# Kernel optimization log

Hardware: AMD Instinct MI355X
Metric: run time of the kernel (lower is better)

The kernel has to match this reference:

```python
import math
import jax, jax.numpy as jnp
import numpy as np

N_KV = 8
GROUP = 4
HEAD_DIM = 128
BATCH = 512
CACHE = 2048
CONTEXT = 4096
NEG_INF = -10000.0


def setup_inputs() -> dict:
    key = jax.random.key(0)
    k = jax.random.split(key, 6)
    queries = jax.random.normal(k[0], (N_KV * GROUP, BATCH, HEAD_DIM), jnp.float32)
    keys = jax.random.normal(k[1], (N_KV, BATCH, HEAD_DIM), jnp.float32)
    key_t_caches = jax.random.normal(k[2], (N_KV, HEAD_DIM, CACHE), jnp.float32)
    values = jax.random.normal(k[3], (N_KV, BATCH, HEAD_DIM), jnp.float32)
    value_caches = jax.random.normal(k[4], (N_KV, CACHE, HEAD_DIM), jnp.float32)
    # causal bias: token b (global position CACHE+b) may attend to positions <= CACHE+b;
    # padded tail [CACHE+BATCH, CONTEXT) is always masked with NEG_INF
    pos = jnp.arange(CONTEXT)[None, :]                       # [1, CONTEXT]
    limit = (CACHE + jnp.arange(BATCH))[:, None]             # [BATCH, 1]
    attn_bias = jnp.where(pos <= limit, 0.0, NEG_INF).astype(jnp.float32)
    kq_scale = jnp.asarray([1.0 / math.sqrt(HEAD_DIM)], jnp.float32)
    return {
        "queries": queries,
        "keys": keys,
        "key_t_caches": key_t_caches,
        "values": values,
        "value_caches": value_caches,
        "attn_bias": attn_bias,
        "kq_scale": kq_scale,
    }


def reference(queries, keys, key_t_caches, values, value_caches, attn_bias, kq_scale):
    n_kv, B, D = keys.shape
    n_heads = queries.shape[0]
    group = n_heads // n_kv
    cache = key_t_caches.shape[-1]
    context = attn_bias.shape[-1]
    pad = context - cache - B

    scaled_keys = keys * kq_scale                            # [kv, B, D]
    scaled_values = jnp.maximum(values, NEG_INF)             # [kv, B, D]

    # pad new keys/values to fill context, then prepend cache (matches torch pad+cat)
    padded_kt = jnp.pad(scaled_keys.transpose(0, 2, 1), ((0, 0), (0, 0), (0, pad)))
    all_keys_t = jnp.concatenate([key_t_caches, padded_kt], axis=-1)   # [kv, D, context]
    padded_v = jnp.pad(scaled_values, ((0, 0), (0, pad), (0, 0)))
    all_values = jnp.concatenate([value_caches, padded_v], axis=1)     # [kv, context, D]

    q = queries.reshape(n_kv, group, B, D)                   # group-major per kv head
    scores = jnp.einsum('kgbd,kdc->kgbc', q, all_keys_t) + attn_bias   # [kv, g, B, context]
    probs = jax.nn.softmax(scores, axis=-1)
    out = jnp.einsum('kgbc,kcd->kgbd', probs, all_values)    # [kv, g, B, D]
    head_outs = out.reshape(n_heads, B, D)
    return head_outs, scaled_keys, scaled_values
```

## Files before the change

### kernel.cpp

```cpp
#include <hip/hip_runtime.h>
#include <hip/hip_bf16.h>

#define NKV 8
#define NHEADS 32
#define HDIM 128
#define BATCH 512
#define CACHE 2048
#define CTX_TOT 2560
#define CT 64
#define SPLITS 4
#define KPITCH 136
#define VPITCH 72
#define PPITCH 72
#define NEG_BIG (-1e30f)

typedef __attribute__((ext_vector_type(8))) _Float16 half8;
typedef __attribute__((ext_vector_type(4))) float floatx4;

__global__ __launch_bounds__(256) void prep(const float* __restrict__ ktc,
                                            const float* __restrict__ vc,
                                            const float* __restrict__ keys,
                                            const float* __restrict__ values,
                                            const float* __restrict__ kq,
                                            float* __restrict__ outk,
                                            float* __restrict__ outv,
                                            _Float16* __restrict__ Kh,
                                            _Float16* __restrict__ Vth) {
    __shared__ float tile[32][33];
    const int bid = blockIdx.x;
    const int t = threadIdx.x;
    const int x = t & 31, y = t >> 5;

    if (bid < 2048) {
        int l = bid;
        int c0 = (l & 63) * 32, d0 = ((l >> 6) & 3) * 32, kv = l >> 8;
        const float* src = ktc + ((size_t)kv * HDIM + d0) * CACHE + c0;
#pragma unroll
        for (int i = 0; i < 4; i++)
            tile[y + 8 * i][x] = src[(size_t)(y + 8 * i) * CACHE + x];
        __syncthreads();
        _Float16* dst = Kh + ((size_t)kv * CTX_TOT + c0) * HDIM + d0;
#pragma unroll
        for (int i = 0; i < 4; i++)
            dst[(size_t)(y + 8 * i) * HDIM + x] = (_Float16)tile[x][y + 8 * i];
    } else if (bid < 4096) {
        int l = bid - 2048;
        int c0 = (l & 63) * 32, d0 = ((l >> 6) & 3) * 32, kv = l >> 8;
        const float* src = vc + ((size_t)kv * CACHE + c0) * HDIM + d0;
#pragma unroll
        for (int i = 0; i < 4; i++)
            tile[y + 8 * i][x] = src[(size_t)(y + 8 * i) * HDIM + x];
        __syncthreads();
        _Float16* dst = Vth + ((size_t)kv * HDIM + d0) * CTX_TOT + c0;
#pragma unroll
        for (int i = 0; i < 4; i++)
            dst[(size_t)(y + 8 * i) * CTX_TOT + x] = (_Float16)tile[x][y + 8 * i];
    } else if (bid < 6144) {
        int i = (bid - 4096) * 256 + t;
        float s = kq[0];
        float v = keys[i] * s;
        outk[i] = v;
        int kv = i >> 16;
        int rem = i & 0xFFFF;
        Kh[((size_t)kv * CTX_TOT + CACHE) * HDIM + rem] = (_Float16)v;
    } else {
        int l = bid - 6144;
        int b0 = (l & 15) * 32, d0 = ((l >> 4) & 3) * 32, kv = l >> 6;
        const float* src = values + ((size_t)kv * BATCH + b0) * HDIM + d0;
        float* dst32 = outv + ((size_t)kv * BATCH + b0) * HDIM + d0;
#pragma unroll
        for (int i = 0; i < 4; i++) {
            float v = fmaxf(src[(size_t)(y + 8 * i) * HDIM + x], -10000.0f);
            tile[y + 8 * i][x] = v;
            dst32[(size_t)(y + 8 * i) * HDIM + x] = v;
        }
        __syncthreads();
        _Float16* dst = Vth + ((size_t)kv * HDIM + d0) * CTX_TOT + CACHE + b0;
#pragma unroll
        for (int i = 0; i < 4; i++)
            dst[(size_t)(y + 8 * i) * CTX_TOT + x] = (_Float16)tile[x][y + 8 * i];
    }
}

__global__ __launch_bounds__(256) void attn_split(const float* __restrict__ q_g,
                                                  const _Float16* __restrict__ Kh,
                                                  const _Float16* __restrict__ Vth,
                                                  float* __restrict__ Opart,
                                                  float* __restrict__ MLpart) {
    __shared__ _Float16 Klds[CT * KPITCH];
    __shared__ _Float16 Vlds[HDIM * VPITCH];
    __shared__ _Float16 Plds[4][16 * PPITCH];

    const int h = blockIdx.x & 31;
    const int qb = blockIdx.x >> 5;
    const int s = blockIdx.y;
    const int kv = h >> 2;
    const int t = threadIdx.x;
    const int wave = t >> 6;
    const int lane = t & 63;
    const int l15 = lane & 15, quad = lane >> 4;

    const float LOG2E = 1.44269504088896340736f;
    const int qrow0 = qb * 64 + wave * 16;
    const float* qp = q_g + ((size_t)h * BATCH + qrow0 + l15) * HDIM + quad * 8;
    half8 qfrag[4];
#pragma unroll
    for (int kb = 0; kb < 4; kb++) {
        const float* p = qp + kb * 32;
        float4 a = *(const float4*)p;
        float4 b = *(const float4*)(p + 4);
        qfrag[kb][0] = (_Float16)(a.x * LOG2E); qfrag[kb][1] = (_Float16)(a.y * LOG2E);
        qfrag[kb][2] = (_Float16)(a.z * LOG2E); qfrag[kb][3] = (_Float16)(a.w * LOG2E);
        qfrag[kb][4] = (_Float16)(b.x * LOG2E); qfrag[kb][5] = (_Float16)(b.y * LOG2E);
        qfrag[kb][6] = (_Float16)(b.z * LOG2E); qfrag[kb][7] = (_Float16)(b.w * LOG2E);
    }

    floatx4 O[8];
#pragma unroll
    for (int nb = 0; nb < 8; nb++) O[nb] = (floatx4){0.f, 0.f, 0.f, 0.f};
    float m_r[4], l_r[4];
#pragma unroll
    for (int r = 0; r < 4; r++) { m_r[r] = NEG_BIG; l_r[r] = 0.f; }

    const int lim_wave = CACHE + qrow0 + 15;
    const int nT = 33 + qb;

    for (int tt = s; tt < nT; tt += SPLITS) {
        const int c0 = tt * CT;
        __syncthreads();
#pragma unroll
        for (int i = 0; i < 4; i++) {
            int ch = t + 256 * i;
            int row = ch >> 4, j = ch & 15;
            uint4 v = *(const uint4*)(Kh + ((size_t)kv * CTX_TOT + c0 + row) * HDIM + j * 8);
            *(uint4*)(&Klds[row * KPITCH + j * 8]) = v;
        }
#pragma unroll
        for (int i = 0; i < 4; i++) {
            int ch = t + 256 * i;
            int row = ch >> 3, j = ch & 7;
            uint4 v = *(const uint4*)(Vth + ((size_t)kv * HDIM + row) * CTX_TOT + c0 + j * 8);
            *(uint4*)(&Vlds[row * VPITCH + j * 8]) = v;
        }
        __syncthreads();

        if (c0 <= lim_wave) {
            floatx4 S[4];
#pragma unroll
            for (int cs = 0; cs < 4; cs++) {
                floatx4 acc = (floatx4){0.f, 0.f, 0.f, 0.f};
                int crow = cs * 16 + l15;
#pragma unroll
                for (int kb = 0; kb < 4; kb++) {
                    half8 kf = *(const half8*)(&Klds[crow * KPITCH + kb * 32 + quad * 8]);
                    acc = __builtin_amdgcn_mfma_f32_16x16x32_f16(qfrag[kb], kf, acc, 0, 0, 0);
                }
                S[cs] = acc;
            }
            if (c0 + CT > CACHE + qb * 64) {
#pragma unroll
                for (int cs = 0; cs < 4; cs++)
#pragma unroll
                    for (int r = 0; r < 4; r++) {
                        int c = c0 + cs * 16 + l15;
                        int brow = qrow0 + quad * 4 + r;
                        if (c > CACHE + brow) S[cs][r] = NEG_BIG;
                    }
            }
            float tmax[4];
#pragma unroll
            for (int r = 0; r < 4; r++)
                tmax[r] = fmaxf(fmaxf(S[0][r], S[1][r]), fmaxf(S[2][r], S[3][r]));
#pragma unroll
            for (int off = 8; off >= 1; off >>= 1)
#pragma unroll
                for (int r = 0; r < 4; r++)
                    tmax[r] = fmaxf(tmax[r], __shfl_xor(tmax[r], off, 64));
            float alpha[4];
#pragma unroll
            for (int r = 0; r < 4; r++) {
                float mn = fmaxf(m_r[r], tmax[r]);
                alpha[r] = __builtin_amdgcn_exp2f(m_r[r] - mn);
                m_r[r] = mn;
                l_r[r] *= alpha[r];
            }
#pragma unroll
            for (int nb = 0; nb < 8; nb++)
#pragma unroll
                for (int r = 0; r < 4; r++) O[nb][r] *= alpha[r];
#pragma unroll
            for (int cs = 0; cs < 4; cs++)
#pragma unroll
                for (int r = 0; r < 4; r++) {
                    float p = __builtin_amdgcn_exp2f(S[cs][r] - m_r[r]);
                    l_r[r] += p;
                    Plds[wave][(quad * 4 + r) * PPITCH + cs * 16 + l15] = (_Float16)p;
                }
#pragma unroll
            for (int kb2 = 0; kb2 < 2; kb2++) {
                half8 pf = *(const half8*)(&Plds[wave][l15 * PPITCH + kb2 * 32 + quad * 8]);
#pragma unroll
                for (int nb = 0; nb < 8; nb++) {
                    half8 vf = *(const half8*)(&Vlds[(nb * 16 + l15) * VPITCH + kb2 * 32 + quad * 8]);
                    O[nb] = __builtin_amdgcn_mfma_f32_16x16x32_f16(pf, vf, O[nb], 0, 0, 0);
                }
            }
        }
    }

#pragma unroll
    for (int off = 8; off >= 1; off >>= 1)
#pragma unroll
        for (int r = 0; r < 4; r++) l_r[r] += __shfl_xor(l_r[r], off, 64);

    const size_t rowbase = (size_t)s * NHEADS * BATCH + (size_t)h * BATCH;
#pragma unroll
    for (int nb = 0; nb < 8; nb++)
#pragma unroll
        for (int r = 0; r < 4; r++) {
            int brow = qrow0 + quad * 4 + r;
            Opart[(rowbase + brow) * HDIM + nb * 16 + l15] = O[nb][r];
        }
    if (l15 == 0) {
#pragma unroll
        for (int r = 0; r < 4; r++) {
            int brow = qrow0 + quad * 4 + r;
            MLpart[(rowbase + brow) * 2 + 0] = m_r[r];
            MLpart[(rowbase + brow) * 2 + 1] = l_r[r];
        }
    }
}

__global__ __launch_bounds__(256) void attn_merge(const float* __restrict__ Opart,
                                                  const float* __restrict__ MLpart,
                                                  float* __restrict__ out) {
    const int t = threadIdx.x;
    const int row = blockIdx.x * 2 + (t >> 7);
    const int d = t & 127;
    const size_t stride = (size_t)NHEADS * BATCH;

    float m0 = MLpart[((size_t)0 * stride + row) * 2];
    float m1 = MLpart[((size_t)1 * stride + row) * 2];
    float m2 = MLpart[((size_t)2 * stride + row) * 2];
    float m3 = MLpart[((size_t)3 * stride + row) * 2];
    float l0 = MLpart[((size_t)0 * stride + row) * 2 + 1];
    float l1 = MLpart[((size_t)1 * stride + row) * 2 + 1];
    float l2 = MLpart[((size_t)2 * stride + row) * 2 + 1];
    float l3 = MLpart[((size_t)3 * stride + row) * 2 + 1];
    float mm = fmaxf(fmaxf(m0, m1), fmaxf(m2, m3));
    float w0 = __builtin_amdgcn_exp2f(m0 - mm);
    float w1 = __builtin_amdgcn_exp2f(m1 - mm);
    float w2 = __builtin_amdgcn_exp2f(m2 - mm);
    float w3 = __builtin_amdgcn_exp2f(m3 - mm);
    float denom = w0 * l0 + w1 * l1 + w2 * l2 + w3 * l3;

    float acc = w0 * Opart[((size_t)0 * stride + row) * HDIM + d]
              + w1 * Opart[((size_t)1 * stride + row) * HDIM + d]
              + w2 * Opart[((size_t)2 * stride + row) * HDIM + d]
              + w3 * Opart[((size_t)3 * stride + row) * HDIM + d];
    out[(size_t)row * HDIM + d] = acc / denom;
}

extern "C" void kernel_launch(void* const* d_in, const int* in_sizes, int n_in,
                              void* d_out, int out_size, void* d_ws, size_t ws_size,
                              hipStream_t stream) {
    const float* queries = (const float*)d_in[0];
    const float* keys    = (const float*)d_in[1];
    const float* ktc     = (const float*)d_in[2];
    const float* values  = (const float*)d_in[3];
    const float* vcache  = (const float*)d_in[4];
    const float* kq      = (const float*)d_in[6];

    float* out     = (float*)d_out;
    float* out_sk  = out + (size_t)NHEADS * BATCH * HDIM;
    float* out_sv  = out_sk + (size_t)NKV * BATCH * HDIM;

    _Float16* Kh   = (_Float16*)d_ws;
    _Float16* Vth  = Kh + (size_t)NKV * CTX_TOT * HDIM;
    float*    Opart = (float*)(Vth + (size_t)NKV * HDIM * CTX_TOT);
    float*    MLpart = Opart + (size_t)SPLITS * NHEADS * BATCH * HDIM;

    prep<<<dim3(6656), dim3(256), 0, stream>>>(ktc, vcache, keys, values, kq,
                                               out_sk, out_sv, Kh, Vth);
    attn_split<<<dim3(256, SPLITS), dim3(256), 0, stream>>>(queries, Kh, Vth, Opart, MLpart);
    attn_merge<<<dim3(8192), dim3(256), 0, stream>>>(Opart, MLpart, out);
}
```

Before: 156.5 us.

## Widen prep tiles, double query rows per attention block, store fp16 partials

The prep kernel now uses larger tiles with float4 loads and half8 stores, which cuts the block count and the number of memory transactions. The attention kernel processes 128 query rows per block, with two 16-row sets per wave, so every K/V tile loaded into LDS is reused twice. Splits go from 4 to 6 to keep the grid filled and launch bounds are set for occupancy 3. Partial outputs are written in fp16 to cut merge traffic, at a small precision cost, and the extra accumulators raise register pressure.

```diff
diff --git a/kernel.cpp b/kernel.cpp
--- a/kernel.cpp
+++ b/kernel.cpp
@@ -8,7 +8,7 @@
 #define CACHE 2048
 #define CTX_TOT 2560
 #define CT 64
-#define SPLITS 4
+#define SPLITS 6
 #define KPITCH 136
 #define VPITCH 72
 #define PPITCH 72
@@ -26,73 +26,101 @@
                                             float* __restrict__ outv,
                                             _Float16* __restrict__ Kh,
                                             _Float16* __restrict__ Vth) {
-    __shared__ float tile[32][33];
+    __shared__ float tile[128 * 33];
     const int bid = blockIdx.x;
     const int t = threadIdx.x;
-    const int x = t & 31, y = t >> 5;
-
-    if (bid < 2048) {
-        int l = bid;
-        int c0 = (l & 63) * 32, d0 = ((l >> 6) & 3) * 32, kv = l >> 8;
-        const float* src = ktc + ((size_t)kv * HDIM + d0) * CACHE + c0;
-#pragma unroll
-        for (int i = 0; i < 4; i++)
-            tile[y + 8 * i][x] = src[(size_t)(y + 8 * i) * CACHE + x];
-        __syncthreads();
-        _Float16* dst = Kh + ((size_t)kv * CTX_TOT + c0) * HDIM + d0;
-#pragma unroll
-        for (int i = 0; i < 4; i++)
-            dst[(size_t)(y + 8 * i) * HDIM + x] = (_Float16)tile[x][y + 8 * i];
-    } else if (bid < 4096) {
-        int l = bid - 2048;
-        int c0 = (l & 63) * 32, d0 = ((l >> 6) & 3) * 32, kv = l >> 8;
-        const float* src = vc + ((size_t)kv * CACHE + c0) * HDIM + d0;
-#pragma unroll
-        for (int i = 0; i < 4; i++)
-            tile[y + 8 * i][x] = src[(size_t)(y + 8 * i) * HDIM + x];
-        __syncthreads();
-        _Float16* dst = Vth + ((size_t)kv * HDIM + d0) * CTX_TOT + c0;
-#pragma unroll
-        for (int i = 0; i < 4; i++)
-            dst[(size_t)(y + 8 * i) * CTX_TOT + x] = (_Float16)tile[x][y + 8 * i];
-    } else if (bid < 6144) {
-        int i = (bid - 4096) * 256 + t;
+
+    if (bid < 512) {
+        int c0 = (bid & 63) * 32, kv = bid >> 6;
+        const float* src = ktc + (size_t)kv * HDIM * CACHE + c0;
+#pragma unroll
+        for (int i = 0; i < 4; i++) {
+            int idx = t + 256 * i;
+            int d = idx >> 3, cc = idx & 7;
+            float4 v = *(const float4*)(src + (size_t)d * CACHE + cc * 4);
+            *(float4*)(&tile[d * 33 + cc * 4]) = v;
+        }
+        __syncthreads();
+        _Float16* dst = Kh + ((size_t)kv * CTX_TOT + c0) * HDIM;
+#pragma unroll
+        for (int i = 0; i < 2; i++) {
+            int c = (t >> 4) + 16 * i, dg = t & 15;
+            half8 o;
+#pragma unroll
+            for (int k = 0; k < 8; k++) o[k] = (_Float16)tile[(dg * 8 + k) * 33 + c];
+            *(half8*)(dst + (size_t)c * HDIM + dg * 8) = o;
+        }
+    } else if (bid < 1024) {
+        int l = bid - 512;
+        int c1 = (l & 15) * 128, d0 = ((l >> 4) & 3) * 32, kv = l >> 6;
+        const float* src = vc + ((size_t)kv * CACHE + c1) * HDIM + d0;
+#pragma unroll
+        for (int i = 0; i < 4; i++) {
+            int idx = t + 256 * i;
+            int c = idx >> 3, dc = idx & 7;
+            float4 v = *(const float4*)(src + (size_t)c * HDIM + dc * 4);
+            *(float4*)(&tile[c * 33 + dc * 4]) = v;
+        }
+        __syncthreads();
+        _Float16* dst = Vth + ((size_t)kv * HDIM + d0) * CTX_TOT + c1;
+#pragma unroll
+        for (int i = 0; i < 2; i++) {
+            int d = (t >> 4) + 16 * i, cg = t & 15;
+            half8 o;
+#pragma unroll
+            for (int k = 0; k < 8; k++) o[k] = (_Float16)tile[(cg * 8 + k) * 33 + d];
+            *(half8*)(dst + (size_t)d * CTX_TOT + cg * 8) = o;
+        }
+    } else if (bid < 1536) {
+        int base = ((bid - 1024) * 256 + t) * 4;
         float s = kq[0];
-        float v = keys[i] * s;
-        outk[i] = v;
-        int kv = i >> 16;
-        int rem = i & 0xFFFF;
-        Kh[((size_t)kv * CTX_TOT + CACHE) * HDIM + rem] = (_Float16)v;
+        float4 v = *(const float4*)(keys + base);
+        v.x *= s; v.y *= s; v.z *= s; v.w *= s;
+        *(float4*)(outk + base) = v;
+        int kv = base >> 16;
+        int rem = base & 0xFFFF;
+        _Float16* dst = Kh + ((size_t)kv * CTX_TOT + CACHE) * HDIM + rem;
+        dst[0] = (_Float16)v.x; dst[1] = (_Float16)v.y;
+        dst[2] = (_Float16)v.z; dst[3] = (_Float16)v.w;
     } else {
-        int l = bid - 6144;
-        int b0 = (l & 15) * 32, d0 = ((l >> 4) & 3) * 32, kv = l >> 6;
-        const float* src = values + ((size_t)kv * BATCH + b0) * HDIM + d0;
-        float* dst32 = outv + ((size_t)kv * BATCH + b0) * HDIM + d0;
-#pragma unroll
-        for (int i = 0; i < 4; i++) {
-            float v = fmaxf(src[(size_t)(y + 8 * i) * HDIM + x], -10000.0f);
-            tile[y + 8 * i][x] = v;
-            dst32[(size_t)(y + 8 * i) * HDIM + x] = v;
-        }
-        __syncthreads();
-        _Float16* dst = Vth + ((size_t)kv * HDIM + d0) * CTX_TOT + CACHE + b0;
-#pragma unroll
-        for (int i = 0; i < 4; i++)
-            dst[(size_t)(y + 8 * i) * CTX_TOT + x] = (_Float16)tile[x][y + 8 * i];
+        int l = bid - 1536;
+        int b1 = (l & 3) * 128, d0 = ((l >> 2) & 3) * 32, kv = l >> 4;
+        const float* src = values + ((size_t)kv * BATCH + b1) * HDIM + d0;
+        float* dst32 = outv + ((size_t)kv * BATCH + b1) * HDIM + d0;
+#pragma unroll
+        for (int i = 0; i < 4; i++) {
+            int idx = t + 256 * i;
+            int b = idx >> 3, dc = idx & 7;
+            float4 v = *(const float4*)(src + (size_t)b * HDIM + dc * 4);
+            v.x = fmaxf(v.x, -10000.0f); v.y = fmaxf(v.y, -10000.0f);
+            v.z = fmaxf(v.z, -10000.0f); v.w = fmaxf(v.w, -10000.0f);
+            *(float4*)(dst32 + (size_t)b * HDIM + dc * 4) = v;
+            *(float4*)(&tile[b * 33 + dc * 4]) = v;
+        }
+        __syncthreads();
+        _Float16* dst = Vth + ((size_t)kv * HDIM + d0) * CTX_TOT + CACHE + b1;
+#pragma unroll
+        for (int i = 0; i < 2; i++) {
+            int d = (t >> 4) + 16 * i, bg = t & 15;
+            half8 o;
+#pragma unroll
+            for (int k = 0; k < 8; k++) o[k] = (_Float16)tile[(bg * 8 + k) * 33 + d];
+            *(half8*)(dst + (size_t)d * CTX_TOT + bg * 8) = o;
+        }
     }
 }
 
-__global__ __launch_bounds__(256) void attn_split(const float* __restrict__ q_g,
-                                                  const _Float16* __restrict__ Kh,
-                                                  const _Float16* __restrict__ Vth,
-                                                  float* __restrict__ Opart,
-                                                  float* __restrict__ MLpart) {
+__global__ __launch_bounds__(256, 3) void attn_split(const float* __restrict__ q_g,
+                                                     const _Float16* __restrict__ Kh,
+                                                     const _Float16* __restrict__ Vth,
+                                                     _Float16* __restrict__ Opart,
+                                                     float* __restrict__ MLpart) {
     __shared__ _Float16 Klds[CT * KPITCH];
     __shared__ _Float16 Vlds[HDIM * VPITCH];
-    __shared__ _Float16 Plds[4][16 * PPITCH];
+    __shared__ _Float16 Plds[4][32 * PPITCH];
 
     const int h = blockIdx.x & 31;
-    const int qb = blockIdx.x >> 5;
+    const int qb2 = blockIdx.x >> 5;
     const int s = blockIdx.y;
     const int kv = h >> 2;
     const int t = threadIdx.x;
@@ -101,29 +129,36 @@
     const int l15 = lane & 15, quad = lane >> 4;
 
     const float LOG2E = 1.44269504088896340736f;
-    const int qrow0 = qb * 64 + wave * 16;
-    const float* qp = q_g + ((size_t)h * BATCH + qrow0 + l15) * HDIM + quad * 8;
-    half8 qfrag[4];
-#pragma unroll
-    for (int kb = 0; kb < 4; kb++) {
-        const float* p = qp + kb * 32;
-        float4 a = *(const float4*)p;
-        float4 b = *(const float4*)(p + 4);
-        qfrag[kb][0] = (_Float16)(a.x * LOG2E); qfrag[kb][1] = (_Float16)(a.y * LOG2E);
-        qfrag[kb][2] = (_Float16)(a.z * LOG2E); qfrag[kb][3] = (_Float16)(a.w * LOG2E);
-        qfrag[kb][4] = (_Float16)(b.x * LOG2E); qfrag[kb][5] = (_Float16)(b.y * LOG2E);
-        qfrag[kb][6] = (_Float16)(b.z * LOG2E); qfrag[kb][7] = (_Float16)(b.w * LOG2E);
-    }
-
-    floatx4 O[8];
-#pragma unroll
-    for (int nb = 0; nb < 8; nb++) O[nb] = (floatx4){0.f, 0.f, 0.f, 0.f};
-    float m_r[4], l_r[4];
-#pragma unroll
-    for (int r = 0; r < 4; r++) { m_r[r] = NEG_BIG; l_r[r] = 0.f; }
-
-    const int lim_wave = CACHE + qrow0 + 15;
-    const int nT = 33 + qb;
+    const int qrow0 = qb2 * 128 + wave * 16;
+
+    half8 qfrag[2][4];
+#pragma unroll
+    for (int hh = 0; hh < 2; hh++) {
+        const float* qp = q_g + ((size_t)h * BATCH + qrow0 + hh * 64 + l15) * HDIM + quad * 8;
+#pragma unroll
+        for (int kb = 0; kb < 4; kb++) {
+            const float* p = qp + kb * 32;
+            float4 a = *(const float4*)p;
+            float4 b = *(const float4*)(p + 4);
+            qfrag[hh][kb][0] = (_Float16)(a.x * LOG2E); qfrag[hh][kb][1] = (_Float16)(a.y * LOG2E);
+            qfrag[hh][kb][2] = (_Float16)(a.z * LOG2E); qfrag[hh][kb][3] = (_Float16)(a.w * LOG2E);
+            qfrag[hh][kb][4] = (_Float16)(b.x * LOG2E); qfrag[hh][kb][5] = (_Float16)(b.y * LOG2E);
+            qfrag[hh][kb][6] = (_Float16)(b.z * LOG2E); qfrag[hh][kb][7] = (_Float16)(b.w * LOG2E);
+        }
+    }
+
+    floatx4 O[2][8];
+#pragma unroll
+    for (int hh = 0; hh < 2; hh++)
+#pragma unroll
+        for (int nb = 0; nb < 8; nb++) O[hh][nb] = (floatx4){0.f, 0.f, 0.f, 0.f};
+    float m_r[2][4], l_r[2][4];
+#pragma unroll
+    for (int hh = 0; hh < 2; hh++)
+#pragma unroll
+        for (int r = 0; r < 4; r++) { m_r[hh][r] = NEG_BIG; l_r[hh][r] = 0.f; }
+
+    const int nT = 34 + 2 * qb2;
 
     for (int tt = s; tt < nT; tt += SPLITS) {
         const int c0 = tt * CT;
@@ -144,94 +179,112 @@
         }
         __syncthreads();
 
-        if (c0 <= lim_wave) {
-            floatx4 S[4];
+        if (c0 <= CACHE + qrow0 + 64 + 15) {
+            floatx4 S[2][4];
 #pragma unroll
             for (int cs = 0; cs < 4; cs++) {
-                floatx4 acc = (floatx4){0.f, 0.f, 0.f, 0.f};
+                floatx4 a0 = (floatx4){0.f, 0.f, 0.f, 0.f};
+                floatx4 a1 = (floatx4){0.f, 0.f, 0.f, 0.f};
                 int crow = cs * 16 + l15;
 #pragma unroll
                 for (int kb = 0; kb < 4; kb++) {
                     half8 kf = *(const half8*)(&Klds[crow * KPITCH + kb * 32 + quad * 8]);
-                    acc = __builtin_amdgcn_mfma_f32_16x16x32_f16(qfrag[kb], kf, acc, 0, 0, 0);
+                    a0 = __builtin_amdgcn_mfma_f32_16x16x32_f16(qfrag[0][kb], kf, a0, 0, 0, 0);
+                    a1 = __builtin_amdgcn_mfma_f32_16x16x32_f16(qfrag[1][kb], kf, a1, 0, 0, 0);
                 }
-                S[cs] = acc;
-            }
-            if (c0 + CT > CACHE + qb * 64) {
-#pragma unroll
-                for (int cs = 0; cs < 4; cs++)
+                S[0][cs] = a0; S[1][cs] = a1;
+            }
+#pragma unroll
+            for (int hh = 0; hh < 2; hh++) {
+                const int qr0h = qrow0 + hh * 64;
+                if (c0 <= CACHE + qr0h + 15) {
+                    if (c0 + CT > CACHE + qr0h) {
+#pragma unroll
+                        for (int cs = 0; cs < 4; cs++)
+#pragma unroll
+                            for (int r = 0; r < 4; r++) {
+                                int c = c0 + cs * 16 + l15;
+                                if (c > CACHE + qr0h + quad * 4 + r) S[hh][cs][r] = NEG_BIG;
+                            }
+                    }
+                    float tmax[4];
+#pragma unroll
+                    for (int r = 0; r < 4; r++)
+                        tmax[r] = fmaxf(fmaxf(S[hh][0][r], S[hh][1][r]),
+                                        fmaxf(S[hh][2][r], S[hh][3][r]));
+#pragma unroll
+                    for (int off = 8; off >= 1; off >>= 1)
+#pragma unroll
+                        for (int r = 0; r < 4; r++)
+                            tmax[r] = fmaxf(tmax[r], __shfl_xor(tmax[r], off, 64));
 #pragma unroll
                     for (int r = 0; r < 4; r++) {
-                        int c = c0 + cs * 16 + l15;
-                        int brow = qrow0 + quad * 4 + r;
-                        if (c > CACHE + brow) S[cs][r] = NEG_BIG;
+                        float mn = fmaxf(m_r[hh][r], tmax[r]);
+                        float alpha = __builtin_amdgcn_exp2f(m_r[hh][r] - mn);
+                        m_r[hh][r] = mn;
+                        l_r[hh][r] *= alpha;
+#pragma unroll
+                        for (int nb = 0; nb < 8; nb++) O[hh][nb][r] *= alpha;
                     }
-            }
-            float tmax[4];
-#pragma unroll
-            for (int r = 0; r < 4; r++)
-                tmax[r] = fmaxf(fmaxf(S[0][r], S[1][r]), fmaxf(S[2][r], S[3][r]));
-#pragma unroll
-            for (int off = 8; off >= 1; off >>= 1)
-#pragma unroll
-                for (int r = 0; r < 4; r++)
-                    tmax[r] = fmaxf(tmax[r], __shfl_xor(tmax[r], off, 64));
-            float alpha[4];
-#pragma unroll
-            for (int r = 0; r < 4; r++) {
-                float mn = fmaxf(m_r[r], tmax[r]);
-                alpha[r] = __builtin_amdgcn_exp2f(m_r[r] - mn);
-                m_r[r] = mn;
-                l_r[r] *= alpha[r];
-            }
-#pragma unroll
-            for (int nb = 0; nb < 8; nb++)
-#pragma unroll
-                for (int r = 0; r < 4; r++) O[nb][r] *= alpha[r];
-#pragma unroll
-            for (int cs = 0; cs < 4; cs++)
-#pragma unroll
-                for (int r = 0; r < 4; r++) {
-                    float p = __builtin_amdgcn_exp2f(S[cs][r] - m_r[r]);
-                    l_r[r] += p;
-                    Plds[wave][(quad * 4 + r) * PPITCH + cs * 16 + l15] = (_Float16)p;
+#pragma unroll
+                    for (int cs = 0; cs < 4; cs++)
+#pragma unroll
+                        for (int r = 0; r < 4; r++) {
+                            float p = __builtin_amdgcn_exp2f(S[hh][cs][r] - m_r[hh][r]);
+                            l_r[hh][r] += p;
+                            Plds[wave][(hh * 16 + quad * 4 + r) * PPITCH + cs * 16 + l15] = (_Float16)p;
+                        }
+                } else {
+#pragma unroll
+                    for (int cs = 0; cs < 4; cs++)
+#pragma unroll
+                        for (int r = 0; r < 4; r++)
+                            Plds[wave][(hh * 16 + quad * 4 + r) * PPITCH + cs * 16 + l15] = (_Float16)0.f;
                 }
+            }
 #pragma unroll
             for (int kb2 = 0; kb2 < 2; kb2++) {
-                half8 pf = *(const half8*)(&Plds[wave][l15 * PPITCH + kb2 * 32 + quad * 8]);
+                half8 pf0 = *(const half8*)(&Plds[wave][l15 * PPITCH + kb2 * 32 + quad * 8]);
+                half8 pf1 = *(const half8*)(&Plds[wave][(16 + l15) * PPITCH + kb2 * 32 + quad * 8]);
 #pragma unroll
                 for (int nb = 0; nb < 8; nb++) {
                     half8 vf = *(const half8*)(&Vlds[(nb * 16 + l15) * VPITCH + kb2 * 32 + quad * 8]);
-                    O[nb] = __builtin_amdgcn_mfma_f32_16x16x32_f16(pf, vf, O[nb], 0, 0, 0);
+                    O[0][nb] = __builtin_amdgcn_mfma_f32_16x16x32_f16(pf0, vf, O[0][nb], 0, 0, 0);
+                    O[1][nb] = __builtin_amdgcn_mfma_f32_16x16x32_f16(pf1, vf, O[1][nb], 0, 0, 0);
                 }
             }
         }
     }
 
 #pragma unroll
-    for (int off = 8; off >= 1; off >>= 1)
-#pragma unroll
-        for (int r = 0; r < 4; r++) l_r[r] += __shfl_xor(l_r[r], off, 64);
+    for (int hh = 0; hh < 2; hh++)
+#pragma unroll
+        for (int off = 8; off >= 1; off >>= 1)
+#pragma unroll
+            for (int r = 0; r < 4; r++) l_r[hh][r] += __shfl_xor(l_r[hh][r], off, 64);
 
     const size_t rowbase = (size_t)s * NHEADS * BATCH + (size_t)h * BATCH;
 #pragma unroll
-    for (int nb = 0; nb < 8; nb++)
-#pragma unroll
-        for (int r = 0; r < 4; r++) {
-            int brow = qrow0 + quad * 4 + r;
-            Opart[(rowbase + brow) * HDIM + nb * 16 + l15] = O[nb][r];
-        }
-    if (l15 == 0) {
-#pragma unroll
-        for (int r = 0; r < 4; r++) {
-            int brow = qrow0 + quad * 4 + r;
-            MLpart[(rowbase + brow) * 2 + 0] = m_r[r];
-            MLpart[(rowbase + brow) * 2 + 1] = l_r[r];
+    for (int hh = 0; hh < 2; hh++) {
+#pragma unroll
+        for (int nb = 0; nb < 8; nb++)
+#pragma unroll
+            for (int r = 0; r < 4; r++) {
+                int brow = qrow0 + hh * 64 + quad * 4 + r;
+                Opart[(rowbase + brow) * HDIM + nb * 16 + l15] = (_Float16)O[hh][nb][r];
+            }
+        if (l15 == 0) {
+#pragma unroll
+            for (int r = 0; r < 4; r++) {
+                int brow = qrow0 + hh * 64 + quad * 4 + r;
+                MLpart[(rowbase + brow) * 2 + 0] = m_r[hh][r];
+                MLpart[(rowbase + brow) * 2 + 1] = l_r[hh][r];
+            }
         }
     }
 }
 
-__global__ __launch_bounds__(256) void attn_merge(const float* __restrict__ Opart,
+__global__ __launch_bounds__(256) void attn_merge(const _Float16* __restrict__ Opart,
                                                   const float* __restrict__ MLpart,
                                                   float* __restrict__ out) {
     const int t = threadIdx.x;
@@ -239,25 +292,21 @@
     const int d = t & 127;
     const size_t stride = (size_t)NHEADS * BATCH;
 
-    float m0 = MLpart[((size_t)0 * stride + row) * 2];
-    float m1 = MLpart[((size_t)1 * stride + row) * 2];
-    float m2 = MLpart[((size_t)2 * stride + row) * 2];
-    float m3 = MLpart[((size_t)3 * stride + row) * 2];
-    float l0 = MLpart[((size_t)0 * stride + row) * 2 + 1];
-    float l1 = MLpart[((size_t)1 * stride + row) * 2 + 1];
-    float l2 = MLpart[((size_t)2 * stride + row) * 2 + 1];
-    float l3 = MLpart[((size_t)3 * stride + row) * 2 + 1];
-    float mm = fmaxf(fmaxf(m0, m1), fmaxf(m2, m3));
-    float w0 = __builtin_amdgcn_exp2f(m0 - mm);
-    float w1 = __builtin_amdgcn_exp2f(m1 - mm);
-    float w2 = __builtin_amdgcn_exp2f(m2 - mm);
-    float w3 = __builtin_amdgcn_exp2f(m3 - mm);
-    float denom = w0 * l0 + w1 * l1 + w2 * l2 + w3 * l3;
-
-    float acc = w0 * Opart[((size_t)0 * stride + row) * HDIM + d]
-              + w1 * Opart[((size_t)1 * stride + row) * HDIM + d]
-              + w2 * Opart[((size_t)2 * stride + row) * HDIM + d]
-              + w3 * Opart[((size_t)3 * stride + row) * HDIM + d];
+    float m[SPLITS], l[SPLITS];
+    float mm = NEG_BIG;
+#pragma unroll
+    for (int s = 0; s < SPLITS; s++) {
+        m[s] = MLpart[((size_t)s * stride + row) * 2];
+        l[s] = MLpart[((size_t)s * stride + row) * 2 + 1];
+        mm = fmaxf(mm, m[s]);
+    }
+    float denom = 0.f, acc = 0.f;
+#pragma unroll
+    for (int s = 0; s < SPLITS; s++) {
+        float w = __builtin_amdgcn_exp2f(m[s] - mm);
+        denom += w * l[s];
+        acc += w * (float)Opart[((size_t)s * stride + row) * HDIM + d];
+    }
     out[(size_t)row * HDIM + d] = acc / denom;
 }
 
@@ -277,11 +326,11 @@
 
     _Float16* Kh   = (_Float16*)d_ws;
     _Float16* Vth  = Kh + (size_t)NKV * CTX_TOT * HDIM;
-    float*    Opart = (float*)(Vth + (size_t)NKV * HDIM * CTX_TOT);
-    float*    MLpart = Opart + (size_t)SPLITS * NHEADS * BATCH * HDIM;
-
-    prep<<<dim3(6656), dim3(256), 0, stream>>>(ktc, vcache, keys, values, kq,
+    _Float16* Opart = Vth + (size_t)NKV * HDIM * CTX_TOT;
+    float*    MLpart = (float*)(Opart + (size_t)SPLITS * NHEADS * BATCH * HDIM);
+
+    prep<<<dim3(1664), dim3(256), 0, stream>>>(ktc, vcache, keys, values, kq,
                                                out_sk, out_sv, Kh, Vth);
-    attn_split<<<dim3(256, SPLITS), dim3(256), 0, stream>>>(queries, Kh, Vth, Opart, MLpart);
+    attn_split<<<dim3(128, SPLITS), dim3(256), 0, stream>>>(queries, Kh, Vth, Opart, MLpart);
     attn_merge<<<dim3(8192), dim3(256), 0, stream>>>(Opart, MLpart, out);
 }
```

Measured after the change: 217.3 us. +38.8%, slower.
